# Kernel optimization log

Hardware: AMD Instinct MI355X
Metric: run time of the kernel (lower is better)

## Reference

```python
import jax, jax.numpy as jnp
import numpy as np
from jax import lax

S = 0.5      # smoothing coefficient (constant in the layer)
EPS = 1e-6   # numerical floor (constant in the layer)


def setup_inputs() -> dict:
    key = jax.random.key(0)
    # [1, F, T] nonnegative spectrogram-like input
    data = jax.random.uniform(key, (1, 1024, 16384), dtype=jnp.float32)
    alpha = jnp.float32(0.98)
    r = jnp.float32(0.5)
    delta = jnp.float32(2.0)
    return {"data": data, "alpha": alpha, "r": r, "delta": delta}


def _ema_over_time(x):
    # x: [F, T]; first-order IIR: m_t = (1-s)*m_{t-1} + s*x_t, m_{-1} = 0
    def step(carry, xt):  # carry, xt: [F]
        m = (1.0 - S) * carry + S * xt
        return m, m
    _, M = lax.scan(step, jnp.zeros(x.shape[0], x.dtype), x.T)  # M: [T, F]
    return M.T  # [F, T]


def reference(data, alpha, r, delta):
    # Original layer computes the smoother M from batch element 0 only
    M = _ema_over_time(data[0])[None]          # [1, F, T]
    Mepow = (M + EPS) ** alpha                  # AGC gain
    pcen = (data / Mepow + delta) ** r - delta ** r
    return pcen
```

## Files before the change

kernel.cpp:

```cpp
#include <hip/hip_runtime.h>


static constexpr int F = 1024;
static constexpr int T = 16384;
static constexpr int C = 16;
static constexpr int BLOCK = 256;
static constexpr int TILE = BLOCK * C;
static constexpr int QT = TILE / 4;
static constexpr float EPS = 1e-6f;

typedef float v4f __attribute__((ext_vector_type(4)));

__device__ __forceinline__ int swz(int q) { return q ^ ((q >> 3) & 7); }

#if __has_builtin(__builtin_amdgcn_logf)
__device__ __forceinline__ float nlog2(float x) { return __builtin_amdgcn_logf(x); }
#else
__device__ __forceinline__ float nlog2(float x) { return log2f(x); }
#endif
#if __has_builtin(__builtin_amdgcn_exp2f)
__device__ __forceinline__ float nexp2(float x) { return __builtin_amdgcn_exp2f(x); }
#else
__device__ __forceinline__ float nexp2(float x) { return exp2f(x); }
#endif
#if __has_builtin(__builtin_amdgcn_sqrtf)
__device__ __forceinline__ float nsqrt(float x) { return __builtin_amdgcn_sqrtf(x); }
#else
__device__ __forceinline__ float nsqrt(float x) { return sqrtf(x); }
#endif

__global__ __launch_bounds__(BLOCK, 8) void pcen_kernel(
    const float* __restrict__ data,
    const float* __restrict__ alpha_p,
    const float* __restrict__ r_p,
    const float* __restrict__ delta_p,
    float* __restrict__ out)
{
  __shared__ v4f lds4[QT];

  const int tid = threadIdx.x;
  const int bid = blockIdx.x;
  const int f = bid >> 2;
  const int h = bid & 3;
  const size_t tilebase = (size_t)f * T + (size_t)h * TILE;
  const size_t tbase = tilebase + (size_t)tid * C;

  float m = 0.0f;
  if ((h | tid) != 0) {
    const v4f* __restrict__ xs =
        reinterpret_cast<const v4f*>(data + tbase - C);
    #pragma unroll
    for (int k = 0; k < 4; ++k) {
      v4f v = xs[k];
      m = 0.5f * (m + v.x);
      m = 0.5f * (m + v.y);
      m = 0.5f * (m + v.z);
      m = 0.5f * (m + v.w);
    }
  }

  const float alpha = alpha_p[0];
  const float r     = r_p[0];
  const float delta = delta_p[0];
  const bool  rhalf = (r == 0.5f);
  const float delta_r = rhalf ? nsqrt(delta) : nexp2(r * nlog2(delta));

  const v4f* __restrict__ xm = reinterpret_cast<const v4f*>(data + tbase);
  v4f res[4];

  #define PCEN_ELEM(XX, OO, POW)                        \
    { m = 0.5f * (m + (XX));                            \
      float lgm = nlog2(m + EPS);                       \
      float inv = nexp2(-alpha * lgm);    \
      float qq  = fmaf((XX), inv, delta);               \
      OO = (POW) - delta_r; }

  if (rhalf) {
    #pragma unroll
    for (int k = 0; k < 4; ++k) {
      v4f v = xm[k];
      v4f o;
      PCEN_ELEM(v.x, o.x, nsqrt(qq));
      PCEN_ELEM(v.y, o.y, nsqrt(qq));
      PCEN_ELEM(v.z, o.z, nsqrt(qq));
      PCEN_ELEM(v.w, o.w, nsqrt(qq));
      res[k] = o;
    }
  } else {
    #pragma unroll
    for (int k = 0; k < 4; ++k) {
      v4f v = xm[k];
      v4f o;
      PCEN_ELEM(v.x, o.x, nexp2(r * nlog2(qq)));
      PCEN_ELEM(v.y, o.y, nexp2(r * nlog2(qq)));
      PCEN_ELEM(v.z, o.z, nexp2(r * nlog2(qq)));
      PCEN_ELEM(v.w, o.w, nexp2(r * nlog2(qq)));
      res[k] = o;
    }
  }
  #undef PCEN_ELEM

  const int tq = tid * 4;
  #pragma unroll
  for (int k = 0; k < 4; ++k) lds4[swz(tq + k)] = res[k];

  __syncthreads();

  v4f* __restrict__ o4 = reinterpret_cast<v4f*>(out + tilebase);
  #pragma unroll
  for (int i = 0; i < 4; ++i) {
    const int p = i * BLOCK + tid;
    __builtin_nontemporal_store(lds4[swz(p)], o4 + p);
  }
}

extern "C" void kernel_launch(void* const* d_in, const int* in_sizes, int n_in,
                              void* d_out, int out_size, void* d_ws, size_t ws_size,
                              hipStream_t stream) {
  const float* data  = (const float*)d_in[0];
  const float* alpha = (const float*)d_in[1];
  const float* r     = (const float*)d_in[2];
  const float* delta = (const float*)d_in[3];
  float* out = (float*)d_out;

  const int grid = F * (T / TILE);
  pcen_kernel<<<dim3(grid), dim3(BLOCK), 0, stream>>>(data, alpha, r, delta, out);
}
```

Before: 25.61 us.

## Replace per-thread strided EMA with wavefront shuffle scan and coalesced loads/stores

Each wavefront now owns a contiguous 1024-element segment and reads it with coalesced float4 loads across lanes. It computes the EMA with an in-register scan: a serial pass within each float4, then a log-step shuffle scan across lanes with power-of-two decay factors, chained between 256-element chunks through a lane-63 broadcast. Results are written directly with coalesced nontemporal stores, which removes the LDS transpose, the block barrier and the per-thread strided 16-element warm-up read. The shuffle scan truncates after three steps, so the EMA only looks back a limited number of lanes. This relies on the 0.5 decay shrinking older terms below float precision, and it adds shuffle instructions to each chunk.

Measured after the change: 25.93 us. About the same (+1.2%).

```diff
diff --git a/kernel.cpp b/kernel.cpp
--- a/kernel.cpp
+++ b/kernel.cpp
@@ -3,15 +3,12 @@
 
 static constexpr int F = 1024;
 static constexpr int T = 16384;
-static constexpr int C = 16;
 static constexpr int BLOCK = 256;
-static constexpr int TILE = BLOCK * C;
-static constexpr int QT = TILE / 4;
+static constexpr int TILE = 4096;
+static constexpr int WSEG = 1024;
 static constexpr float EPS = 1e-6f;
 
 typedef float v4f __attribute__((ext_vector_type(4)));
-
-__device__ __forceinline__ int swz(int q) { return q ^ ((q >> 3) & 7); }
 
 #if __has_builtin(__builtin_amdgcn_logf)
 __device__ __forceinline__ float nlog2(float x) { return __builtin_amdgcn_logf(x); }
@@ -29,6 +26,27 @@
 __device__ __forceinline__ float nsqrt(float x) { return sqrtf(x); }
 #endif
 
+__device__ __forceinline__ float shup(float x, int d, int l) {
+  float t = __shfl_up(x, d, 64);
+  return (l >= d) ? t : 0.0f;
+}
+
+struct Scan { float C0, C1, C2, C3, S; };
+
+__device__ __forceinline__ Scan ema_scan(v4f v, int l) {
+  Scan r;
+  r.C0 = 0.5f * v.x;
+  r.C1 = 0.5f * (r.C0 + v.y);
+  r.C2 = 0.5f * (r.C1 + v.z);
+  r.C3 = 0.5f * (r.C2 + v.w);
+  float S = r.C3;
+  S = fmaf(0x1p-4f,  shup(S, 1, l), S);
+  S = fmaf(0x1p-8f,  shup(S, 2, l), S);
+  S = fmaf(0x1p-16f, shup(S, 4, l), S);
+  r.S = S;
+  return r;
+}
+
 __global__ __launch_bounds__(BLOCK, 8) void pcen_kernel(
     const float* __restrict__ data,
     const float* __restrict__ alpha_p,
@@ -36,82 +54,71 @@
     const float* __restrict__ delta_p,
     float* __restrict__ out)
 {
-  __shared__ v4f lds4[QT];
-
   const int tid = threadIdx.x;
   const int bid = blockIdx.x;
   const int f = bid >> 2;
   const int h = bid & 3;
-  const size_t tilebase = (size_t)f * T + (size_t)h * TILE;
-  const size_t tbase = tilebase + (size_t)tid * C;
+  const int w = tid >> 6;
+  const int l = tid & 63;
+  const size_t base = (size_t)f * T + (size_t)h * TILE + (size_t)w * WSEG;
+  const v4f* __restrict__ g4 = reinterpret_cast<const v4f*>(data + base);
 
-  float m = 0.0f;
-  if ((h | tid) != 0) {
-    const v4f* __restrict__ xs =
-        reinterpret_cast<const v4f*>(data + tbase - C);
-    #pragma unroll
-    for (int k = 0; k < 4; ++k) {
-      v4f v = xs[k];
-      m = 0.5f * (m + v.x);
-      m = 0.5f * (m + v.y);
-      m = 0.5f * (m + v.z);
-      m = 0.5f * (m + v.w);
-    }
-  }
+  v4f v0 = g4[0 * 64 + l];
+  v4f v1 = g4[1 * 64 + l];
+  v4f v2 = g4[2 * 64 + l];
+  v4f v3 = g4[3 * 64 + l];
+  v4f vp = {0.f, 0.f, 0.f, 0.f};
+  if ((h | w) != 0) vp = g4[l - 64];
+
+  Scan p  = ema_scan(vp, l);
+  Scan s0 = ema_scan(v0, l);
+  Scan s1 = ema_scan(v1, l);
+  Scan s2 = ema_scan(v2, l);
+  Scan s3 = ema_scan(v3, l);
+
+  const float seed0 = __shfl(p.S,  63, 64);
+  const float seed1 = __shfl(s0.S, 63, 64);
+  const float seed2 = __shfl(s1.S, 63, 64);
+  const float seed3 = __shfl(s2.S, 63, 64);
+
+  const int ew = 127 - 4 * l;
+  const float pw = (ew > 0) ? __int_as_float(ew << 23) : 0.0f;
 
   const float alpha = alpha_p[0];
   const float r     = r_p[0];
   const float delta = delta_p[0];
   const bool  rhalf = (r == 0.5f);
   const float delta_r = rhalf ? nsqrt(delta) : nexp2(r * nlog2(delta));
+  const float nalpha = -alpha;
 
-  const v4f* __restrict__ xm = reinterpret_cast<const v4f*>(data + tbase);
-  v4f res[4];
+  v4f* __restrict__ o4 = reinterpret_cast<v4f*>(out + base);
 
-  #define PCEN_ELEM(XX, OO, POW)                        \
-    { m = 0.5f * (m + (XX));                            \
-      float lgm = nlog2(m + EPS);                       \
-      float inv = nexp2(-alpha * lgm);    \
-      float qq  = fmaf((XX), inv, delta);               \
-      OO = (POW) - delta_r; }
+  #define PCEN_ONE(XX, MM, OO)                                   \
+    { float lgm = nlog2((MM) + EPS);                             \
+      float inv = nexp2(nalpha * lgm);       \
+      float qq  = fmaf((XX), inv, delta);                        \
+      OO = (rhalf ? nsqrt(qq) : nexp2(r * nlog2(qq))) - delta_r; }
 
-  if (rhalf) {
-    #pragma unroll
-    for (int k = 0; k < 4; ++k) {
-      v4f v = xm[k];
-      v4f o;
-      PCEN_ELEM(v.x, o.x, nsqrt(qq));
-      PCEN_ELEM(v.y, o.y, nsqrt(qq));
-      PCEN_ELEM(v.z, o.z, nsqrt(qq));
-      PCEN_ELEM(v.w, o.w, nsqrt(qq));
-      res[k] = o;
-    }
-  } else {
-    #pragma unroll
-    for (int k = 0; k < 4; ++k) {
-      v4f v = xm[k];
-      v4f o;
-      PCEN_ELEM(v.x, o.x, nexp2(r * nlog2(qq)));
-      PCEN_ELEM(v.y, o.y, nexp2(r * nlog2(qq)));
-      PCEN_ELEM(v.z, o.z, nexp2(r * nlog2(qq)));
-      PCEN_ELEM(v.w, o.w, nexp2(r * nlog2(qq)));
-      res[k] = o;
-    }
-  }
-  #undef PCEN_ELEM
+  #define PCEN_SB(SC, SEED, V, SLOT)                             \
+    { float sl = fmaf(pw, (SEED), shup((SC).S, 1, l));           \
+      float m0 = fmaf(0x1p-1f, sl, (SC).C0);                     \
+      float m1 = fmaf(0x1p-2f, sl, (SC).C1);                     \
+      float m2 = fmaf(0x1p-3f, sl, (SC).C2);                     \
+      float m3 = fmaf(0x1p-4f, sl, (SC).C3);                     \
+      v4f o;                                                     \
+      PCEN_ONE((V).x, m0, o.x);                                  \
+      PCEN_ONE((V).y, m1, o.y);                                  \
+      PCEN_ONE((V).z, m2, o.z);                                  \
+      PCEN_ONE((V).w, m3, o.w);                                  \
+      __builtin_nontemporal_store(o, o4 + (SLOT) * 64 + l); }
 
-  const int tq = tid * 4;
-  #pragma unroll
-  for (int k = 0; k < 4; ++k) lds4[swz(tq + k)] = res[k];
+  PCEN_SB(s0, seed0, v0, 0)
+  PCEN_SB(s1, seed1, v1, 1)
+  PCEN_SB(s2, seed2, v2, 2)
+  PCEN_SB(s3, seed3, v3, 3)
 
-  __syncthreads();
-
-  v4f* __restrict__ o4 = reinterpret_cast<v4f*>(out + tilebase);
-  #pragma unroll
-  for (int i = 0; i < 4; ++i) {
-    const int p = i * BLOCK + tid;
-    __builtin_nontemporal_store(lds4[swz(p)], o4 + p);
-  }
+  #undef PCEN_SB
+  #undef PCEN_ONE
 }
 
 extern "C" void kernel_launch(void* const* d_in, const int* in_sizes, int n_in,
```
